# Kernel tuning notes

Hardware: AMD Instinct MI355X
Metric: run time of the kernel (lower is better)

## Reference

```python
import jax, jax.numpy as jnp
import numpy as np

EMBED_DIM = 512
NUM_HEADS = 8
NUM_RULES = 16
HEAD_DIM = EMBED_DIM // NUM_HEADS


def setup_inputs() -> dict:
    key = jax.random.key(0)
    ks = jax.random.split(key, 10)
    B, S, E, H, R, D = 4, 2048, EMBED_DIM, NUM_HEADS, NUM_RULES, HEAD_DIM
    lim_q = 1.0 / np.sqrt(E)
    lim_v = 1.0 / np.sqrt(E)
    return {
        "query": jax.random.normal(ks[0], (B, S, E), jnp.float32),
        "key": jax.random.normal(ks[1], (B, S, E), jnp.float32),
        "value": jax.random.normal(ks[2], (B, S, E), jnp.float32),
        "Wq": jax.random.uniform(ks[3], (E, E), jnp.float32, -lim_q, lim_q),
        "bq": jax.random.uniform(ks[4], (E,), jnp.float32, -lim_q, lim_q),
        "Wv": jax.random.uniform(ks[5], (E * R, E), jnp.float32, -lim_v, lim_v),
        "bv": jax.random.uniform(ks[6], (E * R,), jnp.float32, -lim_v, lim_v),
        "Wo": jax.random.uniform(ks[7], (E, E), jnp.float32, -lim_q, lim_q),
        "bo": jax.random.uniform(ks[8], (E,), jnp.float32, -lim_q, lim_q),
        "rules_keys": 0.02 * jax.random.normal(ks[9], (H, R, D), jnp.float32),
        "rules_widths": jnp.ones((H, R, D), jnp.float32),
    }


def reference(query, key, value, Wq, bq, Wv, bv, Wo, bo, rules_keys, rules_widths):
    B, S, E = query.shape
    H, R, D = NUM_HEADS, NUM_RULES, HEAD_DIM
    scale = D ** -0.5
    # preprocessing_query: Linear + scale, split heads -> (b, h, s, d)
    q = (query @ Wq.T + bq) * scale
    q = q.reshape(B, S, H, D).transpose(0, 2, 1, 3)
    # custom_distance (l1): |q - rule_key| broadcast over rules -> (b, h, s, r, d)
    diff = jnp.abs(q[:, :, :, None, :] - rules_keys[None, :, None, :, :])
    # get_z_values: z = mean_d( -0.5 * (diff / width)^2 ) -> (b, h, s, r)
    z = -0.5 * jnp.mean(jnp.square(diff / rules_widths[None, :, None, :, :]), axis=-1)
    # softmax over rules (last dim), dropout is identity (p=0)
    attn = jax.nn.softmax(z, axis=-1)  # (b, h, s, r)
    # preprocessing_value: Linear(E -> E*R) + scale, 'b s (h d r) -> b s h d r'
    v = (value @ Wv.T + bv) * scale
    v = v.reshape(B, S, H, D, R)
    # Fnn_output = attn * v summed over rules -> (b, s, h, d)
    out = jnp.einsum("bhsr,bshdr->bshd", attn, v)
    # torch: (b,s,h,d).transpose(1,2).contiguous().view(b, -1, h*d)
    out = out.transpose(0, 2, 1, 3).reshape(B, -1, H * D)
    return out @ Wo.T + bo
```

## Files before the change

kernel.cpp:

```cpp
#include <hip/hip_runtime.h>
#include <stdint.h>

#define TOKENS 8192
#define EDIM 512
#define HNUM 8
#define RNUM 16
#define DDIM 64
#define KDIM 512

typedef short v8s __attribute__((ext_vector_type(8)));
typedef float v4f __attribute__((ext_vector_type(4)));

__device__ inline float b2f(unsigned short u) {
    union { unsigned int i; float f; } c; c.i = ((unsigned int)u) << 16; return c.f;
}
__device__ inline unsigned short f2b(float f) {
    union { float f; unsigned int i; } c; c.f = f;
    unsigned int i = c.i + 0x7fffu + ((c.i >> 16) & 1u);
    return (unsigned short)(i >> 16);
}

#define GLD16(dst, src) \
    __builtin_amdgcn_global_load_lds((__attribute__((address_space(1))) void*)(src), \
                                     (__attribute__((address_space(3))) void*)(dst), 16, 0, 0)

__global__ __launch_bounds__(256)
void cvt5(const float* __restrict__ s0, const float* __restrict__ s1,
          const float* __restrict__ s2, const float* __restrict__ s3,
          const float* __restrict__ s4,
          unsigned short* __restrict__ d0, unsigned short* __restrict__ d1,
          unsigned short* __restrict__ d2, unsigned short* __restrict__ d3,
          unsigned short* __restrict__ d4,
          int n0, int n1, int n2, int n3, int n4)
{
    const float* s; unsigned short* d; int n;
    switch (blockIdx.y) {
        case 0: s = s0; d = d0; n = n0; break;
        case 1: s = s1; d = d1; n = n1; break;
        case 2: s = s2; d = d2; n = n2; break;
        case 3: s = s3; d = d3; n = n3; break;
        default: s = s4; d = d4; n = n4; break;
    }
    size_t base = (size_t)blockIdx.x * 2048 + (size_t)threadIdx.x * 8;
    if (base >= (size_t)n) return;
    const float4* sp = (const float4*)(s + base);
    float4 f0 = sp[0], f1 = sp[1];
    v8s o;
    o[0] = (short)f2b(f0.x); o[1] = (short)f2b(f0.y);
    o[2] = (short)f2b(f0.z); o[3] = (short)f2b(f0.w);
    o[4] = (short)f2b(f1.x); o[5] = (short)f2b(f1.y);
    o[6] = (short)f2b(f1.z); o[7] = (short)f2b(f1.w);
    *(v8s*)(d + base) = o;
}

template <int MODE>
__global__ __launch_bounds__(256, 4)
void gemm64(const unsigned short* __restrict__ A,
            const unsigned short* __restrict__ B,
            const float* __restrict__ bias,
            float* __restrict__ outF,
            unsigned short* __restrict__ outH)
{
    __shared__ unsigned short As[64 * 32];
    __shared__ unsigned short Bs[64 * 32];

    const int tid  = threadIdx.x;
    const int w    = tid >> 6;
    const int lane = tid & 63;
    const int quad = lane >> 4;
    const int l16  = lane & 15;
    const int wm   = w >> 1, wn = w & 1;
    const int m0   = blockIdx.x * 64;
    const int n0   = blockIdx.y * 64;

    v4f acc[2][2];
#pragma unroll
    for (int i = 0; i < 2; ++i)
#pragma unroll
        for (int j = 0; j < 2; ++j)
            acc[i][j] = (v4f){0.f, 0.f, 0.f, 0.f};

    for (int kt = 0; kt < KDIM / 32; ++kt) {
        int c = w * 64 + lane;
        const unsigned short* sa = A + (size_t)(m0 + (c >> 2)) * KDIM + kt * 32 + (c & 3) * 8;
        GLD16(&As[w * 512], sa);
        const unsigned short* sb = B + (size_t)(n0 + (c >> 2)) * KDIM + kt * 32 + (c & 3) * 8;
        GLD16(&Bs[w * 512], sb);
        __syncthreads();

        v8s af[2], bf[2];
#pragma unroll
        for (int mt = 0; mt < 2; ++mt)
            af[mt] = *(const v8s*)&As[(wm * 32 + mt * 16 + l16) * 32 + quad * 8];
#pragma unroll
        for (int nt = 0; nt < 2; ++nt)
            bf[nt] = *(const v8s*)&Bs[(wn * 32 + nt * 16 + l16) * 32 + quad * 8];
#pragma unroll
        for (int mt = 0; mt < 2; ++mt)
#pragma unroll
            for (int nt = 0; nt < 2; ++nt)
                acc[mt][nt] = __builtin_amdgcn_mfma_f32_16x16x32_bf16(af[mt], bf[nt], acc[mt][nt], 0, 0, 0);
        __syncthreads();
    }

#pragma unroll
    for (int mt = 0; mt < 2; ++mt)
#pragma unroll
        for (int nt = 0; nt < 2; ++nt) {
            int col = n0 + wn * 32 + nt * 16 + l16;
            float bb = bias[col];
#pragma unroll
            for (int rg = 0; rg < 4; ++rg) {
                int row = m0 + wm * 32 + mt * 16 + quad * 4 + rg;
                float v = acc[mt][nt][rg] + bb;
                if (MODE == 0) outH[(size_t)row * EDIM + col] = f2b(v * 0.125f);
                else           outF[(size_t)row * EDIM + col] = v;
            }
        }
}

__device__ __forceinline__ v8s ldfrag(const unsigned short* base, int r, int g) {
    return *(const v8s*)(base + ((r >> 1) << 6) + ((((((r & 1) << 2)) | g) ^ ((r >> 1) & 7)) << 3));
}

#define MEMBAR asm volatile("" ::: "memory")
#define BARX do { MEMBAR; __builtin_amdgcn_s_barrier(); MEMBAR; } while (0)
#define BARL do { MEMBAR; asm volatile("s_waitcnt lgkmcnt(0)" ::: "memory"); \
                  __builtin_amdgcn_s_barrier(); MEMBAR; } while (0)
#define WAITV(n) asm volatile("s_waitcnt vmcnt(" #n ")" ::: "memory")

#define STAGE_T(bufp, gptr, grow0, k0s) do { \
    const unsigned short* s_ = (gptr) + (size_t)((grow0) + (w << 5) + rloc) * KDIM + (k0s) + gidx * 8; \
    GLD16((bufp) + (w << 10), s_); \
    GLD16((bufp) + (w << 10) + 512, s_ + 16 * KDIM); \
} while (0)

__global__ __launch_bounds__(512, 2)
void gemm_v(const unsigned short* __restrict__ A,
            const unsigned short* __restrict__ B,
            const float* __restrict__ bias,
            unsigned short* __restrict__ outH,
            const float* __restrict__ attn)
{
    __shared__ unsigned short As3[3][8192];
    __shared__ unsigned short Bs3[3][8192];
    __shared__ unsigned short Os[4096];

    const int tid  = threadIdx.x;
    const int w    = tid >> 6;
    const int lane = tid & 63;
    const int quad = lane >> 4;
    const int l16  = lane & 15;
    const int wm   = w >> 2;
    const int wn   = w & 3;
    const int su   = (lane & 7) ^ ((lane >> 3) & 7);
    const int rloc = ((lane >> 3) << 1) | (su >> 2);
    const int gidx = su & 3;

    const int c  = blockIdx.x & 7;
    const int j  = blockIdx.x >> 3;
    const int mb = ((c & 3) << 3) | (j & 7);
    const int ng = ((c >> 2) << 2) | (j >> 3);
    const int m0  = mb << 8;
    const int n0b = ng << 10;

    v4f acc[4][4][2];
#pragma unroll
    for (int q = 0; q < 4; ++q)
#pragma unroll
        for (int mi = 0; mi < 4; ++mi)
#pragma unroll
            for (int ni = 0; ni < 2; ++ni)
                acc[q][mi][ni] = (v4f){0.f, 0.f, 0.f, 0.f};

    const int h  = m0 >> 10;
    const int d0 = (m0 >> 4) & 63;

    STAGE_T(&As3[0][0], A, m0, 0);
    STAGE_T(&Bs3[0][0], B, n0b, 0);
    STAGE_T(&As3[1][0], A, m0, 32);
    STAGE_T(&Bs3[1][0], B, n0b, 32);
    WAITV(4);
    BARX;

    int cur = 0;
#pragma unroll 1
    for (int G = 0; G < 64; ++G) {
        const unsigned short* abase = (cur == 0) ? &As3[0][0] : (cur == 1) ? &As3[1][0] : &As3[2][0];
        const unsigned short* bbase = (cur == 0) ? &Bs3[0][0] : (cur == 1) ? &Bs3[1][0] : &Bs3[2][0];

        v8s af[8], bf[4];
#pragma unroll
        for (int mq = 0; mq < 2; ++mq)
#pragma unroll
            for (int mi = 0; mi < 4; ++mi)
                af[mq * 4 + mi] = ldfrag(abase, mq * 128 + wm * 64 + mi * 16 + l16, quad);
#pragma unroll
        for (int nq = 0; nq < 2; ++nq)
#pragma unroll
            for (int ni = 0; ni < 2; ++ni)
                bf[nq * 2 + ni] = ldfrag(bbase, nq * 128 + wn * 32 + ni * 16 + l16, quad);

        if (G < 62) {
            const int G2  = G + 2;
            const int stg = (cur == 0) ? 2 : cur - 1;
            unsigned short* sa = (stg == 0) ? &As3[0][0] : (stg == 1) ? &As3[1][0] : &As3[2][0];
            unsigned short* sb = (stg == 0) ? &Bs3[0][0] : (stg == 1) ? &Bs3[1][0] : &Bs3[2][0];
            const int k0s = (G2 & 15) * 32;
            const int n0s = n0b + ((G2 >> 4) << 8);
            STAGE_T(sa, A, m0, k0s);
            STAGE_T(sb, B, n0s, k0s);
        }

        __builtin_amdgcn_s_setprio(1);
#pragma unroll
        for (int mq = 0; mq < 2; ++mq)
#pragma unroll
            for (int nq = 0; nq < 2; ++nq)
#pragma unroll
                for (int mi = 0; mi < 4; ++mi)
#pragma unroll
                    for (int ni = 0; ni < 2; ++ni)
                        acc[mq * 2 + nq][mi][ni] = __builtin_amdgcn_mfma_f32_16x16x32_bf16(
                            af[mq * 4 + mi], bf[nq * 2 + ni], acc[mq * 2 + nq][mi][ni], 0, 0, 0);
        __builtin_amdgcn_s_setprio(0);

        if (G < 62) { WAITV(4); } else { WAITV(0); }
        BARX;

        if ((G & 15) == 15) {
            const int n0t = n0b + ((G >> 4) << 8);
#pragma unroll
            for (int mq = 0; mq < 2; ++mq)
#pragma unroll
                for (int nq = 0; nq < 2; ++nq)
#pragma unroll
                    for (int mi = 0; mi < 4; ++mi) {
                        float4 bias4 = *(const float4*)&bias[m0 + mq * 128 + wm * 64 + mi * 16 + quad * 4];
#pragma unroll
                        for (int ni = 0; ni < 2; ++ni) {
                            int tloc  = nq * 128 + wn * 32 + ni * 16 + l16;
                            float4 av = *(const float4*)&attn[(size_t)(n0t + tloc) * (HNUM * RNUM) + h * RNUM + quad * 4];
                            v4f a = acc[mq * 2 + nq][mi][ni];
                            float val = (a[0] + bias4.x) * av.x + (a[1] + bias4.y) * av.y
                                      + (a[2] + bias4.z) * av.z + (a[3] + bias4.w) * av.w;
                            val += __shfl_xor(val, 16);
                            val += __shfl_xor(val, 32);
                            if (quad == 0)
                                Os[tloc * 16 + (mq * 8 + wm * 4 + mi)] = f2b(val * 0.125f);
                        }
                    }
            BARL;
            {
                int tl = tid >> 1, hf = tid & 1;
                int sg = n0t + tl;
                int g  = (sg >> 11) * 2048 + h * 256 + ((sg & 2047) >> 3);
                int jx = (sg & 7) * 64 + d0 + hf * 8;
                *(v8s*)&outH[(size_t)g * EDIM + jx] = *(const v8s*)&Os[tl * 16 + hf * 8];
            }
            if (G < 63) {
#pragma unroll
                for (int q = 0; q < 4; ++q)
#pragma unroll
                    for (int mi = 0; mi < 4; ++mi)
#pragma unroll
                        for (int ni = 0; ni < 2; ++ni)
                            acc[q][mi][ni] = (v4f){0.f, 0.f, 0.f, 0.f};
            }
        }
        cur = (cur == 2) ? 0 : cur + 1;
    }
}

#define RST 72
__global__ __launch_bounds__(256)
void rules_softmax(const unsigned short* __restrict__ q,
                   const float* __restrict__ rk,
                   const float* __restrict__ rw,
                   float* __restrict__ attn)
{
    __shared__ float ql[16 * RST];
    __shared__ float rkl[16 * RST];
    __shared__ float iwl[16 * RST];
    const int h   = blockIdx.y;
    const int t0  = blockIdx.x * 16;
    const int tid = threadIdx.x;

#pragma unroll
    for (int i = 0; i < 4; ++i) {
        int jj = tid + i * 256;
        int r = jj >> 6, d = jj & 63;
        rkl[r * RST + d] = rk[h * (RNUM * DDIM) + jj];
        float wv = rw[h * (RNUM * DDIM) + jj];
        iwl[r * RST + d] = 1.0f / (wv * wv);
    }
    {
        int jj = tid * 4;
        int row = jj >> 6, d = jj & 63;
        const unsigned short* src = q + (size_t)(t0 + row) * EDIM + h * DDIM + d;
        unsigned short u0 = src[0], u1 = src[1], u2 = src[2], u3 = src[3];
        ql[row * RST + d + 0] = b2f(u0);
        ql[row * RST + d + 1] = b2f(u1);
        ql[row * RST + d + 2] = b2f(u2);
        ql[row * RST + d + 3] = b2f(u3);
    }
    __syncthreads();

    const int tl = tid >> 4;
    const int r  = tid & 15;
    const float* qrow = &ql[tl * RST];
    const float* krow = &rkl[r * RST];
    const float* wrow = &iwl[r * RST];
    float z = 0.f;
#pragma unroll
    for (int d4 = 0; d4 < 16; ++d4) {
        float4 qv = *(const float4*)&qrow[d4 * 4];
        float4 kv = *(const float4*)&krow[d4 * 4];
        float4 wv = *(const float4*)&wrow[d4 * 4];
        float a0 = qv.x - kv.x; z += a0 * a0 * wv.x;
        float a1 = qv.y - kv.y; z += a1 * a1 * wv.y;
        float a2 = qv.z - kv.z; z += a2 * a2 * wv.z;
        float a3 = qv.w - kv.w; z += a3 * a3 * wv.w;
    }
    z *= (-0.5f / 64.f);
    float mx = z;
#pragma unroll
    for (int s = 1; s < 16; s <<= 1) mx = fmaxf(mx, __shfl_xor(mx, s));
    float e = __expf(z - mx);
    float sum = e;
#pragma unroll
    for (int s = 1; s < 16; s <<= 1) sum += __shfl_xor(sum, s);
    attn[(size_t)(t0 + tl) * (HNUM * RNUM) + h * RNUM + r] = e / sum;
}

extern "C" void kernel_launch(void* const* d_in, const int* in_sizes, int n_in,
                              void* d_out, int out_size, void* d_ws, size_t ws_size,
                              hipStream_t stream) {
    const float* query = (const float*)d_in[0];
    const float* value = (const float*)d_in[2];
    const float* Wq = (const float*)d_in[3];
    const float* bq = (const float*)d_in[4];
    const float* Wv = (const float*)d_in[5];
    const float* bv = (const float*)d_in[6];
    const float* Wo = (const float*)d_in[7];
    const float* bo = (const float*)d_in[8];
    const float* rk = (const float*)d_in[9];
    const float* rw = (const float*)d_in[10];

    char* ws = (char*)d_ws;
    unsigned short* qbf  = (unsigned short*)(ws);
    unsigned short* vbf  = (unsigned short*)(ws + (size_t)( 8 << 20));
    unsigned short* Wqb  = (unsigned short*)(ws + (size_t)(16 << 20));
    unsigned short* Wvb  = (unsigned short*)(ws + (size_t)(17 << 20));
    unsigned short* Wob  = (unsigned short*)(ws + (size_t)(25 << 20));
    unsigned short* out1 = (unsigned short*)(ws + (size_t)(26 << 20));
    unsigned short* qf   = (unsigned short*)(ws + (size_t)(34 << 20));
    float* attn          = (float*)(ws + (size_t)(42 << 20));

    dim3 blk(256);
    cvt5<<<dim3(2048, 5), blk, 0, stream>>>(query, value, Wv, Wq, Wo,
                                            qbf, vbf, Wvb, Wqb, Wob,
                                            TOKENS * EDIM, TOKENS * EDIM, EDIM * RNUM * EDIM,
                                            EDIM * EDIM, EDIM * EDIM);
    gemm64<0><<<dim3(TOKENS / 64, EDIM / 64), blk, 0, stream>>>(qbf, Wqb, bq, nullptr, qf);
    rules_softmax<<<dim3(TOKENS / 16, HNUM), blk, 0, stream>>>(qf, rk, rw, attn);
    gemm_v<<<dim3(256), dim3(512), 0, stream>>>(Wvb, vbf, bv, out1, attn);
    gemm64<2><<<dim3(TOKENS / 64, EDIM / 64), blk, 0, stream>>>(out1, Wob, bo, (float*)d_out, nullptr);
}
```

Baseline: 226.2 us.

## Fuse rules softmax into Q projection GEMM and enlarge output GEMM tiles

The query projection GEMM now computes each 64-column head tile into shared memory as fp32 and evaluates the rule distances and softmax in its epilogue. This removes the separate rules_softmax kernel and the bf16 q round-trip through global memory. The output projection moves to a 128x128 tile kernel with 4x4 MFMA fragments per wave to improve data reuse. The costs are more shared memory and registers per block, and fewer blocks for the final GEMM (256 blocks).

```diff
diff --git a/kernel.cpp b/kernel.cpp
--- a/kernel.cpp
+++ b/kernel.cpp
@@ -53,16 +53,21 @@
     *(v8s*)(d + base) = o;
 }
 
-template <int MODE>
+#define RST 72
+
 __global__ __launch_bounds__(256, 4)
-void gemm64(const unsigned short* __restrict__ A,
-            const unsigned short* __restrict__ B,
-            const float* __restrict__ bias,
-            float* __restrict__ outF,
-            unsigned short* __restrict__ outH)
+void gemm64q(const unsigned short* __restrict__ A,
+             const unsigned short* __restrict__ B,
+             const float* __restrict__ bias,
+             const float* __restrict__ rk,
+             const float* __restrict__ rw,
+             float* __restrict__ attn)
 {
     __shared__ unsigned short As[64 * 32];
     __shared__ unsigned short Bs[64 * 32];
+    __shared__ float qs[64 * 68];
+    __shared__ float rkl[16 * RST];
+    __shared__ float iwl[16 * RST];
 
     const int tid  = threadIdx.x;
     const int w    = tid >> 6;
@@ -71,7 +76,17 @@
     const int l16  = lane & 15;
     const int wm   = w >> 1, wn = w & 1;
     const int m0   = blockIdx.x * 64;
-    const int n0   = blockIdx.y * 64;
+    const int h    = blockIdx.y;
+    const int n0   = h * 64;
+
+#pragma unroll
+    for (int i = 0; i < 4; ++i) {
+        int jj = tid + i * 256;
+        int r = jj >> 6, d = jj & 63;
+        rkl[r * RST + d] = rk[h * (RNUM * DDIM) + jj];
+        float wv = rw[h * (RNUM * DDIM) + jj];
+        iwl[r * RST + d] = 1.0f / (wv * wv);
+    }
 
     v4f acc[2][2];
 #pragma unroll
@@ -107,16 +122,44 @@
     for (int mt = 0; mt < 2; ++mt)
 #pragma unroll
         for (int nt = 0; nt < 2; ++nt) {
-            int col = n0 + wn * 32 + nt * 16 + l16;
-            float bb = bias[col];
+            int col = wn * 32 + nt * 16 + l16;
+            float bb = bias[n0 + col];
 #pragma unroll
             for (int rg = 0; rg < 4; ++rg) {
-                int row = m0 + wm * 32 + mt * 16 + quad * 4 + rg;
-                float v = acc[mt][nt][rg] + bb;
-                if (MODE == 0) outH[(size_t)row * EDIM + col] = f2b(v * 0.125f);
-                else           outF[(size_t)row * EDIM + col] = v;
+                int row = wm * 32 + mt * 16 + quad * 4 + rg;
+                qs[row * 68 + col] = (acc[mt][nt][rg] + bb) * 0.125f;
             }
         }
+    __syncthreads();
+
+    const int tl = tid >> 4;
+    const int r  = tid & 15;
+    const float* krow = &rkl[r * RST];
+    const float* wrow = &iwl[r * RST];
+#pragma unroll
+    for (int p = 0; p < 4; ++p) {
+        const float* qrow = &qs[(p * 16 + tl) * 68];
+        float z = 0.f;
+#pragma unroll
+        for (int d4 = 0; d4 < 16; ++d4) {
+            float4 qv = *(const float4*)&qrow[d4 * 4];
+            float4 kv = *(const float4*)&krow[d4 * 4];
+            float4 wv = *(const float4*)&wrow[d4 * 4];
+            float a0 = qv.x - kv.x; z += a0 * a0 * wv.x;
+            float a1 = qv.y - kv.y; z += a1 * a1 * wv.y;
+            float a2 = qv.z - kv.z; z += a2 * a2 * wv.z;
+            float a3 = qv.w - kv.w; z += a3 * a3 * wv.w;
+        }
+        z *= (-0.5f / 64.f);
+        float mx = z;
+#pragma unroll
+        for (int s = 1; s < 16; s <<= 1) mx = fmaxf(mx, __shfl_xor(mx, s));
+        float e = __expf(z - mx);
+        float sum = e;
+#pragma unroll
+        for (int s = 1; s < 16; s <<= 1) sum += __shfl_xor(sum, s);
+        attn[(size_t)(m0 + p * 16 + tl) * (HNUM * RNUM) + h * RNUM + r] = e / sum;
+    }
 }
 
 __device__ __forceinline__ v8s ldfrag(const unsigned short* base, int r, int g) {
@@ -272,65 +315,70 @@
     }
 }
 
-#define RST 72
-__global__ __launch_bounds__(256)
-void rules_softmax(const unsigned short* __restrict__ q,
-                   const float* __restrict__ rk,
-                   const float* __restrict__ rw,
-                   float* __restrict__ attn)
+__global__ __launch_bounds__(256, 2)
+void gemm128o(const unsigned short* __restrict__ A,
+              const unsigned short* __restrict__ B,
+              const float* __restrict__ bias,
+              float* __restrict__ outF)
 {
-    __shared__ float ql[16 * RST];
-    __shared__ float rkl[16 * RST];
-    __shared__ float iwl[16 * RST];
-    const int h   = blockIdx.y;
-    const int t0  = blockIdx.x * 16;
-    const int tid = threadIdx.x;
-
-#pragma unroll
-    for (int i = 0; i < 4; ++i) {
-        int jj = tid + i * 256;
-        int r = jj >> 6, d = jj & 63;
-        rkl[r * RST + d] = rk[h * (RNUM * DDIM) + jj];
-        float wv = rw[h * (RNUM * DDIM) + jj];
-        iwl[r * RST + d] = 1.0f / (wv * wv);
-    }
-    {
-        int jj = tid * 4;
-        int row = jj >> 6, d = jj & 63;
-        const unsigned short* src = q + (size_t)(t0 + row) * EDIM + h * DDIM + d;
-        unsigned short u0 = src[0], u1 = src[1], u2 = src[2], u3 = src[3];
-        ql[row * RST + d + 0] = b2f(u0);
-        ql[row * RST + d + 1] = b2f(u1);
-        ql[row * RST + d + 2] = b2f(u2);
-        ql[row * RST + d + 3] = b2f(u3);
-    }
-    __syncthreads();
-
-    const int tl = tid >> 4;
-    const int r  = tid & 15;
-    const float* qrow = &ql[tl * RST];
-    const float* krow = &rkl[r * RST];
-    const float* wrow = &iwl[r * RST];
-    float z = 0.f;
-#pragma unroll
-    for (int d4 = 0; d4 < 16; ++d4) {
-        float4 qv = *(const float4*)&qrow[d4 * 4];
-        float4 kv = *(const float4*)&krow[d4 * 4];
-        float4 wv = *(const float4*)&wrow[d4 * 4];
-        float a0 = qv.x - kv.x; z += a0 * a0 * wv.x;
-        float a1 = qv.y - kv.y; z += a1 * a1 * wv.y;
-        float a2 = qv.z - kv.z; z += a2 * a2 * wv.z;
-        float a3 = qv.w - kv.w; z += a3 * a3 * wv.w;
-    }
-    z *= (-0.5f / 64.f);
-    float mx = z;
-#pragma unroll
-    for (int s = 1; s < 16; s <<= 1) mx = fmaxf(mx, __shfl_xor(mx, s));
-    float e = __expf(z - mx);
-    float sum = e;
-#pragma unroll
-    for (int s = 1; s < 16; s <<= 1) sum += __shfl_xor(sum, s);
-    attn[(size_t)(t0 + tl) * (HNUM * RNUM) + h * RNUM + r] = e / sum;
+    __shared__ unsigned short As[128 * 32];
+    __shared__ unsigned short Bs[128 * 32];
+
+    const int tid  = threadIdx.x;
+    const int w    = tid >> 6;
+    const int lane = tid & 63;
+    const int quad = lane >> 4;
+    const int l16  = lane & 15;
+    const int wm   = w >> 1, wn = w & 1;
+    const int m0   = blockIdx.x * 128;
+    const int n0   = blockIdx.y * 128;
+
+    v4f acc[4][4];
+#pragma unroll
+    for (int i = 0; i < 4; ++i)
+#pragma unroll
+        for (int j = 0; j < 4; ++j)
+            acc[i][j] = (v4f){0.f, 0.f, 0.f, 0.f};
+
+    for (int kt = 0; kt < KDIM / 32; ++kt) {
+#pragma unroll
+        for (int p = 0; p < 2; ++p) {
+            int cb = w * 128 + p * 64;
+            int c  = cb + lane;
+            const unsigned short* sa = A + (size_t)(m0 + (c >> 2)) * KDIM + kt * 32 + (c & 3) * 8;
+            GLD16(&As[cb * 8], sa);
+            const unsigned short* sb = B + (size_t)(n0 + (c >> 2)) * KDIM + kt * 32 + (c & 3) * 8;
+            GLD16(&Bs[cb * 8], sb);
+        }
+        __syncthreads();
+
+        v8s af[4], bf[4];
+#pragma unroll
+        for (int mt = 0; mt < 4; ++mt)
+            af[mt] = *(const v8s*)&As[(wm * 64 + mt * 16 + l16) * 32 + quad * 8];
+#pragma unroll
+        for (int nt = 0; nt < 4; ++nt)
+            bf[nt] = *(const v8s*)&Bs[(wn * 64 + nt * 16 + l16) * 32 + quad * 8];
+#pragma unroll
+        for (int mt = 0; mt < 4; ++mt)
+#pragma unroll
+            for (int nt = 0; nt < 4; ++nt)
+                acc[mt][nt] = __builtin_amdgcn_mfma_f32_16x16x32_bf16(af[mt], bf[nt], acc[mt][nt], 0, 0, 0);
+        __syncthreads();
+    }
+
+#pragma unroll
+    for (int mt = 0; mt < 4; ++mt)
+#pragma unroll
+        for (int nt = 0; nt < 4; ++nt) {
+            int col = n0 + wn * 64 + nt * 16 + l16;
+            float bb = bias[col];
+#pragma unroll
+            for (int rg = 0; rg < 4; ++rg) {
+                int row = m0 + wm * 64 + mt * 16 + quad * 4 + rg;
+                outF[(size_t)row * EDIM + col] = acc[mt][nt][rg] + bb;
+            }
+        }
 }
 
 extern "C" void kernel_launch(void* const* d_in, const int* in_sizes, int n_in,
@@ -354,7 +402,6 @@
     unsigned short* Wvb  = (unsigned short*)(ws + (size_t)(17 << 20));
     unsigned short* Wob  = (unsigned short*)(ws + (size_t)(25 << 20));
     unsigned short* out1 = (unsigned short*)(ws + (size_t)(26 << 20));
-    unsigned short* qf   = (unsigned short*)(ws + (size_t)(34 << 20));
     float* attn          = (float*)(ws + (size_t)(42 << 20));
 
     dim3 blk(256);
@@ -362,8 +409,7 @@
                                             qbf, vbf, Wvb, Wqb, Wob,
                                             TOKENS * EDIM, TOKENS * EDIM, EDIM * RNUM * EDIM,
                                             EDIM * EDIM, EDIM * EDIM);
-    gemm64<0><<<dim3(TOKENS / 64, EDIM / 64), blk, 0, stream>>>(qbf, Wqb, bq, nullptr, qf);
-    rules_softmax<<<dim3(TOKENS / 16, HNUM), blk, 0, stream>>>(qf, rk, rw, attn);
+    gemm64q<<<dim3(TOKENS / 64, HNUM), blk, 0, stream>>>(qbf, Wqb, bq, rk, rw, attn);
     gemm_v<<<dim3(256), dim3(512), 0, stream>>>(Wvb, vbf, bv, out1, attn);
-    gemm64<2><<<dim3(TOKENS / 64, EDIM / 64), blk, 0, stream>>>(out1, Wob, bo, (float*)d_out, nullptr);
-}
+    gemm128o<<<dim3(TOKENS / 128, EDIM / 128), blk, 0, stream>>>(out1, Wob, bo, (float*)d_out);
+}
```

New measurement: 369.8 us. 1.63x slower.

## Switch value GEMM to 32x32x16 MFMA with half-tile double-buffered staging

Applied to the files above, without the earlier changes.

Rewrites the fused value-projection GEMM to use 32x32x16 bf16 MFMA instead of 16x16x32, with K-steps of 64 and a two-buffer LDS scheme where each half of the M/N tile is refilled separately. The loaded tile gets a new XOR swizzle and the attention-weighted epilogue is adapted to the 32x32 accumulator layout. The aim is fewer MFMA issues, fewer fragment loads per FLOP and fewer barriers per unit of K. The trade-offs are a finer-grained prefetch schedule that may expose load latency, and more LDS in use (64KB plus output staging), which could limit occupancy.

```diff
diff --git a/kernel.cpp b/kernel.cpp
--- a/kernel.cpp
+++ b/kernel.cpp
@@ -10,6 +10,7 @@
 
 typedef short v8s __attribute__((ext_vector_type(8)));
 typedef float v4f __attribute__((ext_vector_type(4)));
+typedef float v16f __attribute__((ext_vector_type(16)));
 
 __device__ inline float b2f(unsigned short u) {
     union { unsigned int i; float f; } c; c.i = ((unsigned int)u) << 16; return c.f;
@@ -120,7 +121,7 @@
 }
 
 __device__ __forceinline__ v8s ldfrag(const unsigned short* base, int r, int g) {
-    return *(const v8s*)(base + ((r >> 1) << 6) + ((((((r & 1) << 2)) | g) ^ ((r >> 1) & 7)) << 3));
+    return *(const v8s*)(base + (r << 6) + ((g ^ (r & 7)) << 3));
 }
 
 #define MEMBAR asm volatile("" ::: "memory")
@@ -129,10 +130,11 @@
                   __builtin_amdgcn_s_barrier(); MEMBAR; } while (0)
 #define WAITV(n) asm volatile("s_waitcnt vmcnt(" #n ")" ::: "memory")
 
-#define STAGE_T(bufp, gptr, grow0, k0s) do { \
-    const unsigned short* s_ = (gptr) + (size_t)((grow0) + (w << 5) + rloc) * KDIM + (k0s) + gidx * 8; \
-    GLD16((bufp) + (w << 10), s_); \
-    GLD16((bufp) + (w << 10) + 512, s_ + 16 * KDIM); \
+#define STAGE_H(ldsArr, bufi, half_, gptr, rowbase, kof) do { \
+    const unsigned short* s_ = (gptr) + (size_t)((rowbase) + (half_) * 128 + (w << 4) + rsub) * KDIM \
+                               + (kof) + (gsw << 3); \
+    GLD16(&ldsArr[bufi][(half_) * 8192 + (w << 10)], s_); \
+    GLD16(&ldsArr[bufi][(half_) * 8192 + (w << 10) + 512], s_ + 8 * KDIM); \
 } while (0)
 
 __global__ __launch_bounds__(512, 2)
@@ -142,20 +144,19 @@
             unsigned short* __restrict__ outH,
             const float* __restrict__ attn)
 {
-    __shared__ unsigned short As3[3][8192];
-    __shared__ unsigned short Bs3[3][8192];
+    __shared__ unsigned short As[2][16384];
+    __shared__ unsigned short Bs[2][16384];
     __shared__ unsigned short Os[4096];
 
     const int tid  = threadIdx.x;
     const int w    = tid >> 6;
     const int lane = tid & 63;
-    const int quad = lane >> 4;
-    const int l16  = lane & 15;
+    const int l31  = lane & 31;
+    const int hi   = lane >> 5;
     const int wm   = w >> 2;
     const int wn   = w & 3;
-    const int su   = (lane & 7) ^ ((lane >> 3) & 7);
-    const int rloc = ((lane >> 3) << 1) | (su >> 2);
-    const int gidx = su & 3;
+    const int rsub = lane >> 3;
+    const int gsw  = (lane & 7) ^ rsub;
 
     const int c  = blockIdx.x & 7;
     const int j  = blockIdx.x >> 3;
@@ -164,111 +165,145 @@
     const int m0  = mb << 8;
     const int n0b = ng << 10;
 
-    v4f acc[4][4][2];
-#pragma unroll
-    for (int q = 0; q < 4; ++q)
-#pragma unroll
-        for (int mi = 0; mi < 4; ++mi)
-#pragma unroll
-            for (int ni = 0; ni < 2; ++ni)
-                acc[q][mi][ni] = (v4f){0.f, 0.f, 0.f, 0.f};
+    v16f acc[2][2][2];
+#pragma unroll
+    for (int mq = 0; mq < 2; ++mq)
+#pragma unroll
+        for (int mi = 0; mi < 2; ++mi)
+#pragma unroll
+            for (int nq = 0; nq < 2; ++nq)
+#pragma unroll
+                for (int e = 0; e < 16; ++e)
+                    acc[mq][mi][nq][e] = 0.f;
 
     const int h  = m0 >> 10;
     const int d0 = (m0 >> 4) & 63;
 
-    STAGE_T(&As3[0][0], A, m0, 0);
-    STAGE_T(&Bs3[0][0], B, n0b, 0);
-    STAGE_T(&As3[1][0], A, m0, 32);
-    STAGE_T(&Bs3[1][0], B, n0b, 32);
+    STAGE_H(As, 0, 0, A, m0, 0);
+    STAGE_H(Bs, 0, 0, B, n0b, 0);
+    STAGE_H(As, 0, 1, A, m0, 0);
+    STAGE_H(Bs, 0, 1, B, n0b, 0);
+    STAGE_H(As, 1, 0, A, m0, 64);
+    STAGE_H(Bs, 1, 1, B, n0b, 64);
     WAITV(4);
     BARX;
 
-    int cur = 0;
 #pragma unroll 1
-    for (int G = 0; G < 64; ++G) {
-        const unsigned short* abase = (cur == 0) ? &As3[0][0] : (cur == 1) ? &As3[1][0] : &As3[2][0];
-        const unsigned short* bbase = (cur == 0) ? &Bs3[0][0] : (cur == 1) ? &Bs3[1][0] : &Bs3[2][0];
-
-        v8s af[8], bf[4];
+    for (int nt = 0; nt < 4; ++nt) {
+        const int n0t = n0b + (nt << 8);
+#pragma unroll
+        for (int T8 = 0; T8 < 8; ++T8) {
+            const int T   = nt * 8 + T8;
+            const int cur = T8 & 1, ob = cur ^ 1;
+            const unsigned short* abase = &As[cur][0];
+            const unsigned short* bbase = &Bs[cur][0];
+            const int t1 = T + 1, t2 = T + 2;
+
+            v8s af[2][4], bf[2][4];
+
+#pragma unroll
+            for (int mi = 0; mi < 2; ++mi)
+#pragma unroll
+                for (int kt = 0; kt < 4; ++kt)
+                    af[mi][kt] = ldfrag(abase, wm * 64 + mi * 32 + l31, kt * 2 + hi);
+#pragma unroll
+            for (int nq = 0; nq < 2; ++nq)
+#pragma unroll
+                for (int kt = 0; kt < 4; ++kt)
+                    bf[nq][kt] = ldfrag(bbase, nq * 128 + wn * 32 + l31, kt * 2 + hi);
+            if (t1 < 32) {
+                const int kof1 = (t1 & 7) << 6;
+                STAGE_H(As, ob, 1, A, m0, kof1);
+                STAGE_H(Bs, ob, 0, B, n0b + ((t1 >> 3) << 8), kof1);
+            }
+            __builtin_amdgcn_s_setprio(1);
+#pragma unroll
+            for (int kt = 0; kt < 4; ++kt)
+#pragma unroll
+                for (int mi = 0; mi < 2; ++mi)
+#pragma unroll
+                    for (int nq = 0; nq < 2; ++nq)
+                        acc[0][mi][nq] = __builtin_amdgcn_mfma_f32_32x32x16_bf16(
+                            af[mi][kt], bf[nq][kt], acc[0][mi][nq], 0, 0, 0);
+            __builtin_amdgcn_s_setprio(0);
+            BARX;
+
+#pragma unroll
+            for (int mi = 0; mi < 2; ++mi)
+#pragma unroll
+                for (int kt = 0; kt < 4; ++kt)
+                    af[mi][kt] = ldfrag(abase, 128 + wm * 64 + mi * 32 + l31, kt * 2 + hi);
+            if (t2 < 32) {
+                const int kof2 = (t2 & 7) << 6;
+                STAGE_H(As, cur, 0, A, m0, kof2);
+                STAGE_H(Bs, cur, 1, B, n0b + ((t2 >> 3) << 8), kof2);
+            }
+            __builtin_amdgcn_s_setprio(1);
+#pragma unroll
+            for (int kt = 0; kt < 4; ++kt)
+#pragma unroll
+                for (int mi = 0; mi < 2; ++mi)
+#pragma unroll
+                    for (int nq = 0; nq < 2; ++nq)
+                        acc[1][mi][nq] = __builtin_amdgcn_mfma_f32_32x32x16_bf16(
+                            af[mi][kt], bf[nq][kt], acc[1][mi][nq], 0, 0, 0);
+            __builtin_amdgcn_s_setprio(0);
+            if (T < 30) { WAITV(4); } else { WAITV(0); }
+            BARX;
+        }
+
 #pragma unroll
         for (int mq = 0; mq < 2; ++mq)
 #pragma unroll
-            for (int mi = 0; mi < 4; ++mi)
-                af[mq * 4 + mi] = ldfrag(abase, mq * 128 + wm * 64 + mi * 16 + l16, quad);
-#pragma unroll
-        for (int nq = 0; nq < 2; ++nq)
-#pragma unroll
-            for (int ni = 0; ni < 2; ++ni)
-                bf[nq * 2 + ni] = ldfrag(bbase, nq * 128 + wn * 32 + ni * 16 + l16, quad);
-
-        if (G < 62) {
-            const int G2  = G + 2;
-            const int stg = (cur == 0) ? 2 : cur - 1;
-            unsigned short* sa = (stg == 0) ? &As3[0][0] : (stg == 1) ? &As3[1][0] : &As3[2][0];
-            unsigned short* sb = (stg == 0) ? &Bs3[0][0] : (stg == 1) ? &Bs3[1][0] : &Bs3[2][0];
-            const int k0s = (G2 & 15) * 32;
-            const int n0s = n0b + ((G2 >> 4) << 8);
-            STAGE_T(sa, A, m0, k0s);
-            STAGE_T(sb, B, n0s, k0s);
+            for (int mi = 0; mi < 2; ++mi) {
+                const int mbase = m0 + mq * 128 + wm * 64 + mi * 32;
+                float4 b40 = *(const float4*)&bias[mbase + 0  + hi * 4];
+                float4 b41 = *(const float4*)&bias[mbase + 8  + hi * 4];
+                float4 b42 = *(const float4*)&bias[mbase + 16 + hi * 4];
+                float4 b43 = *(const float4*)&bias[mbase + 24 + hi * 4];
+#pragma unroll
+                for (int nq = 0; nq < 2; ++nq) {
+                    const int tloc = nq * 128 + wn * 32 + l31;
+                    const size_t t = (size_t)(n0t + tloc);
+                    float4 alo = *(const float4*)&attn[t * (HNUM * RNUM) + h * RNUM + hi * 4];
+                    float4 ahi = *(const float4*)&attn[t * (HNUM * RNUM) + h * RNUM + 8 + hi * 4];
+                    v16f a = acc[mq][mi][nq];
+                    float v0 = (a[0]  + b40.x) * alo.x + (a[1]  + b40.y) * alo.y
+                             + (a[2]  + b40.z) * alo.z + (a[3]  + b40.w) * alo.w
+                             + (a[4]  + b41.x) * ahi.x + (a[5]  + b41.y) * ahi.y
+                             + (a[6]  + b41.z) * ahi.z + (a[7]  + b41.w) * ahi.w;
+                    float v1 = (a[8]  + b42.x) * alo.x + (a[9]  + b42.y) * alo.y
+                             + (a[10] + b42.z) * alo.z + (a[11] + b42.w) * alo.w
+                             + (a[12] + b43.x) * ahi.x + (a[13] + b43.y) * ahi.y
+                             + (a[14] + b43.z) * ahi.z + (a[15] + b43.w) * ahi.w;
+                    v0 += __shfl_xor(v0, 32);
+                    v1 += __shfl_xor(v1, 32);
+                    if (hi == 0) {
+                        const int dl = mq * 8 + wm * 4 + mi * 2;
+                        Os[tloc * 16 + dl]     = f2b(v0 * 0.125f);
+                        Os[tloc * 16 + dl + 1] = f2b(v1 * 0.125f);
+                    }
+                }
+            }
+        BARL;
+        {
+            int tl = tid >> 1, hf = tid & 1;
+            int sg = n0t + tl;
+            int g  = (sg >> 11) * 2048 + h * 256 + ((sg & 2047) >> 3);
+            int jx = (sg & 7) * 64 + d0 + hf * 8;
+            *(v8s*)&outH[(size_t)g * EDIM + jx] = *(const v8s*)&Os[tl * 16 + hf * 8];
         }
-
-        __builtin_amdgcn_s_setprio(1);
-#pragma unroll
-        for (int mq = 0; mq < 2; ++mq)
-#pragma unroll
-            for (int nq = 0; nq < 2; ++nq)
-#pragma unroll
-                for (int mi = 0; mi < 4; ++mi)
-#pragma unroll
-                    for (int ni = 0; ni < 2; ++ni)
-                        acc[mq * 2 + nq][mi][ni] = __builtin_amdgcn_mfma_f32_16x16x32_bf16(
-                            af[mq * 4 + mi], bf[nq * 2 + ni], acc[mq * 2 + nq][mi][ni], 0, 0, 0);
-        __builtin_amdgcn_s_setprio(0);
-
-        if (G < 62) { WAITV(4); } else { WAITV(0); }
-        BARX;
-
-        if ((G & 15) == 15) {
-            const int n0t = n0b + ((G >> 4) << 8);
+        if (nt < 3) {
 #pragma unroll
             for (int mq = 0; mq < 2; ++mq)
 #pragma unroll
-                for (int nq = 0; nq < 2; ++nq)
-#pragma unroll
-                    for (int mi = 0; mi < 4; ++mi) {
-                        float4 bias4 = *(const float4*)&bias[m0 + mq * 128 + wm * 64 + mi * 16 + quad * 4];
-#pragma unroll
-                        for (int ni = 0; ni < 2; ++ni) {
-                            int tloc  = nq * 128 + wn * 32 + ni * 16 + l16;
-                            float4 av = *(const float4*)&attn[(size_t)(n0t + tloc) * (HNUM * RNUM) + h * RNUM + quad * 4];
-                            v4f a = acc[mq * 2 + nq][mi][ni];
-                            float val = (a[0] + bias4.x) * av.x + (a[1] + bias4.y) * av.y
-                                      + (a[2] + bias4.z) * av.z + (a[3] + bias4.w) * av.w;
-                            val += __shfl_xor(val, 16);
-                            val += __shfl_xor(val, 32);
-                            if (quad == 0)
-                                Os[tloc * 16 + (mq * 8 + wm * 4 + mi)] = f2b(val * 0.125f);
-                        }
-                    }
-            BARL;
-            {
-                int tl = tid >> 1, hf = tid & 1;
-                int sg = n0t + tl;
-                int g  = (sg >> 11) * 2048 + h * 256 + ((sg & 2047) >> 3);
-                int jx = (sg & 7) * 64 + d0 + hf * 8;
-                *(v8s*)&outH[(size_t)g * EDIM + jx] = *(const v8s*)&Os[tl * 16 + hf * 8];
-            }
-            if (G < 63) {
-#pragma unroll
-                for (int q = 0; q < 4; ++q)
-#pragma unroll
-                    for (int mi = 0; mi < 4; ++mi)
-#pragma unroll
-                        for (int ni = 0; ni < 2; ++ni)
-                            acc[q][mi][ni] = (v4f){0.f, 0.f, 0.f, 0.f};
-            }
+                for (int mi = 0; mi < 2; ++mi)
+#pragma unroll
+                    for (int nq = 0; nq < 2; ++nq)
+#pragma unroll
+                        for (int e = 0; e < 16; ++e)
+                            acc[mq][mi][nq][e] = 0.f;
         }
-        cur = (cur == 2) ? 0 : cur + 1;
     }
 }
 
```

Result: slower. 251.5 us (+11.2%).

## Deepen gemm_v pipeline to four LDS stages with register fragment double-buffering

Applied to the files above, without the earlier changes.

The value-projection GEMM goes from a 3-stage to a 4-stage LDS ring and preloads the next k-step's A/B fragments into a second register set while the current MFMAs run. The loop is unrolled by two so the fragment buffers and stage indices stay static. The goal is to hide LDS read latency and global-load latency behind the MFMA work. In exchange, LDS use roughly doubles past what two blocks per CU can share, so launch bounds drop to one block per CU and occupancy falls. Register pressure also rises.

```diff
diff --git a/kernel.cpp b/kernel.cpp
--- a/kernel.cpp
+++ b/kernel.cpp
@@ -135,15 +135,43 @@
     GLD16((bufp) + (w << 10) + 512, s_ + 16 * KDIM); \
 } while (0)
 
-__global__ __launch_bounds__(512, 2)
+#define PREF(afr, bfr, ab, bb) do { \
+    _Pragma("unroll") \
+    for (int mq = 0; mq < 2; ++mq) \
+        _Pragma("unroll") \
+        for (int mi = 0; mi < 4; ++mi) \
+            afr[mq * 4 + mi] = ldfrag(ab, mq * 128 + wm * 64 + mi * 16 + l16, quad); \
+    _Pragma("unroll") \
+    for (int nq = 0; nq < 2; ++nq) \
+        _Pragma("unroll") \
+        for (int ni = 0; ni < 2; ++ni) \
+            bfr[nq * 2 + ni] = ldfrag(bb, nq * 128 + wn * 32 + ni * 16 + l16, quad); \
+} while (0)
+
+#define MFMA32(afr, bfr) do { \
+    __builtin_amdgcn_s_setprio(1); \
+    _Pragma("unroll") \
+    for (int mq = 0; mq < 2; ++mq) \
+        _Pragma("unroll") \
+        for (int nq = 0; nq < 2; ++nq) \
+            _Pragma("unroll") \
+            for (int mi = 0; mi < 4; ++mi) \
+                _Pragma("unroll") \
+                for (int ni = 0; ni < 2; ++ni) \
+                    acc[mq * 2 + nq][mi][ni] = __builtin_amdgcn_mfma_f32_16x16x32_bf16( \
+                        afr[mq * 4 + mi], bfr[nq * 2 + ni], acc[mq * 2 + nq][mi][ni], 0, 0, 0); \
+    __builtin_amdgcn_s_setprio(0); \
+} while (0)
+
+__global__ __launch_bounds__(512, 1)
 void gemm_v(const unsigned short* __restrict__ A,
             const unsigned short* __restrict__ B,
             const float* __restrict__ bias,
             unsigned short* __restrict__ outH,
             const float* __restrict__ attn)
 {
-    __shared__ unsigned short As3[3][8192];
-    __shared__ unsigned short Bs3[3][8192];
+    __shared__ unsigned short As3[4][8192];
+    __shared__ unsigned short Bs3[4][8192];
     __shared__ unsigned short Os[4096];
 
     const int tid  = threadIdx.x;
@@ -176,99 +204,96 @@
     const int h  = m0 >> 10;
     const int d0 = (m0 >> 4) & 63;
 
+    v8s afA[8], bfA[4], afB[8], bfB[4];
+
     STAGE_T(&As3[0][0], A, m0, 0);
     STAGE_T(&Bs3[0][0], B, n0b, 0);
     STAGE_T(&As3[1][0], A, m0, 32);
     STAGE_T(&Bs3[1][0], B, n0b, 32);
+    STAGE_T(&As3[2][0], A, m0, 64);
+    STAGE_T(&Bs3[2][0], B, n0b, 64);
     WAITV(4);
     BARX;
-
-    int cur = 0;
+    PREF(afA, bfA, &As3[0][0], &Bs3[0][0]);
+
 #pragma unroll 1
-    for (int G = 0; G < 64; ++G) {
-        const unsigned short* abase = (cur == 0) ? &As3[0][0] : (cur == 1) ? &As3[1][0] : &As3[2][0];
-        const unsigned short* bbase = (cur == 0) ? &Bs3[0][0] : (cur == 1) ? &Bs3[1][0] : &Bs3[2][0];
-
-        v8s af[8], bf[4];
-#pragma unroll
-        for (int mq = 0; mq < 2; ++mq)
-#pragma unroll
-            for (int mi = 0; mi < 4; ++mi)
-                af[mq * 4 + mi] = ldfrag(abase, mq * 128 + wm * 64 + mi * 16 + l16, quad);
-#pragma unroll
-        for (int nq = 0; nq < 2; ++nq)
-#pragma unroll
-            for (int ni = 0; ni < 2; ++ni)
-                bf[nq * 2 + ni] = ldfrag(bbase, nq * 128 + wn * 32 + ni * 16 + l16, quad);
-
-        if (G < 62) {
-            const int G2  = G + 2;
-            const int stg = (cur == 0) ? 2 : cur - 1;
-            unsigned short* sa = (stg == 0) ? &As3[0][0] : (stg == 1) ? &As3[1][0] : &As3[2][0];
-            unsigned short* sb = (stg == 0) ? &Bs3[0][0] : (stg == 1) ? &Bs3[1][0] : &Bs3[2][0];
-            const int k0s = (G2 & 15) * 32;
-            const int n0s = n0b + ((G2 >> 4) << 8);
-            STAGE_T(sa, A, m0, k0s);
-            STAGE_T(sb, B, n0s, k0s);
+    for (int gp = 0; gp < 32; ++gp) {
+        const int p = gp & 1;
+        {
+            const int G = gp * 2;
+            const int preb = p ? 3 : 1;
+            const int stgb = p ? 1 : 3;
+            PREF(afB, bfB, &As3[preb][0], &Bs3[preb][0]);
+            if (G <= 60) {
+                const int e3 = G + 3;
+                STAGE_T(&As3[stgb][0], A, m0, (e3 & 15) * 32);
+                STAGE_T(&Bs3[stgb][0], B, n0b + ((e3 >> 4) << 8), (e3 & 15) * 32);
+                MFMA32(afA, bfA);
+                WAITV(4);
+            } else {
+                MFMA32(afA, bfA);
+                WAITV(0);
+            }
+            BARX;
         }
-
-        __builtin_amdgcn_s_setprio(1);
-#pragma unroll
-        for (int mq = 0; mq < 2; ++mq)
-#pragma unroll
-            for (int nq = 0; nq < 2; ++nq)
-#pragma unroll
-                for (int mi = 0; mi < 4; ++mi)
-#pragma unroll
-                    for (int ni = 0; ni < 2; ++ni)
-                        acc[mq * 2 + nq][mi][ni] = __builtin_amdgcn_mfma_f32_16x16x32_bf16(
-                            af[mq * 4 + mi], bf[nq * 2 + ni], acc[mq * 2 + nq][mi][ni], 0, 0, 0);
-        __builtin_amdgcn_s_setprio(0);
-
-        if (G < 62) { WAITV(4); } else { WAITV(0); }
-        BARX;
-
-        if ((G & 15) == 15) {
-            const int n0t = n0b + ((G >> 4) << 8);
-#pragma unroll
-            for (int mq = 0; mq < 2; ++mq)
-#pragma unroll
-                for (int nq = 0; nq < 2; ++nq)
-#pragma unroll
-                    for (int mi = 0; mi < 4; ++mi) {
-                        float4 bias4 = *(const float4*)&bias[m0 + mq * 128 + wm * 64 + mi * 16 + quad * 4];
-#pragma unroll
-                        for (int ni = 0; ni < 2; ++ni) {
-                            int tloc  = nq * 128 + wn * 32 + ni * 16 + l16;
-                            float4 av = *(const float4*)&attn[(size_t)(n0t + tloc) * (HNUM * RNUM) + h * RNUM + quad * 4];
-                            v4f a = acc[mq * 2 + nq][mi][ni];
-                            float val = (a[0] + bias4.x) * av.x + (a[1] + bias4.y) * av.y
-                                      + (a[2] + bias4.z) * av.z + (a[3] + bias4.w) * av.w;
-                            val += __shfl_xor(val, 16);
-                            val += __shfl_xor(val, 32);
-                            if (quad == 0)
-                                Os[tloc * 16 + (mq * 8 + wm * 4 + mi)] = f2b(val * 0.125f);
+        {
+            const int G = gp * 2 + 1;
+            const int preb = p ? 0 : 2;
+            const int stgb = p ? 2 : 0;
+            if (G < 63) PREF(afA, bfA, &As3[preb][0], &Bs3[preb][0]);
+            if (G <= 60) {
+                const int e3 = G + 3;
+                STAGE_T(&As3[stgb][0], A, m0, (e3 & 15) * 32);
+                STAGE_T(&Bs3[stgb][0], B, n0b + ((e3 >> 4) << 8), (e3 & 15) * 32);
+                MFMA32(afB, bfB);
+                WAITV(4);
+            } else {
+                MFMA32(afB, bfB);
+                WAITV(0);
+            }
+            BARX;
+
+            if ((G & 15) == 15) {
+                const int n0t = n0b + ((G >> 4) << 8);
+#pragma unroll
+                for (int mq = 0; mq < 2; ++mq)
+#pragma unroll
+                    for (int nq = 0; nq < 2; ++nq)
+#pragma unroll
+                        for (int mi = 0; mi < 4; ++mi) {
+                            float4 bias4 = *(const float4*)&bias[m0 + mq * 128 + wm * 64 + mi * 16 + quad * 4];
+#pragma unroll
+                            for (int ni = 0; ni < 2; ++ni) {
+                                int tloc  = nq * 128 + wn * 32 + ni * 16 + l16;
+                                float4 av = *(const float4*)&attn[(size_t)(n0t + tloc) * (HNUM * RNUM) + h * RNUM + quad * 4];
+                                v4f a = acc[mq * 2 + nq][mi][ni];
+                                float val = (a[0] + bias4.x) * av.x + (a[1] + bias4.y) * av.y
+                                          + (a[2] + bias4.z) * av.z + (a[3] + bias4.w) * av.w;
+                                val += __shfl_xor(val, 16);
+                                val += __shfl_xor(val, 32);
+                                if (quad == 0)
+                                    Os[tloc * 16 + (mq * 8 + wm * 4 + mi)] = f2b(val * 0.125f);
+                            }
                         }
-                    }
-            BARL;
-            {
-                int tl = tid >> 1, hf = tid & 1;
-                int sg = n0t + tl;
-                int g  = (sg >> 11) * 2048 + h * 256 + ((sg & 2047) >> 3);
-                int jx = (sg & 7) * 64 + d0 + hf * 8;
-                *(v8s*)&outH[(size_t)g * EDIM + jx] = *(const v8s*)&Os[tl * 16 + hf * 8];
-            }
-            if (G < 63) {
-#pragma unroll
-                for (int q = 0; q < 4; ++q)
-#pragma unroll
-                    for (int mi = 0; mi < 4; ++mi)
-#pragma unroll
-                        for (int ni = 0; ni < 2; ++ni)
-                            acc[q][mi][ni] = (v4f){0.f, 0.f, 0.f, 0.f};
+                BARL;
+                {
+                    int tl = tid >> 1, hf = tid & 1;
+                    int sg = n0t + tl;
+                    int g  = (sg >> 11) * 2048 + h * 256 + ((sg & 2047) >> 3);
+                    int jx = (sg & 7) * 64 + d0 + hf * 8;
+                    *(v8s*)&outH[(size_t)g * EDIM + jx] = *(const v8s*)&Os[tl * 16 + hf * 8];
+                }
+                if (G < 63) {
+#pragma unroll
+                    for (int q = 0; q < 4; ++q)
+#pragma unroll
+                        for (int mi = 0; mi < 4; ++mi)
+#pragma unroll
+                            for (int ni = 0; ni < 2; ++ni)
+                                acc[q][mi][ni] = (v4f){0.f, 0.f, 0.f, 0.f};
+                }
             }
         }
-        cur = (cur == 2) ? 0 : cur + 1;
     }
 }
 
```

Measured after the change: 884.8 us. 3.91x slower.
